# Kernel tuning notes

Measured on AMD Instinct MI355X. Metric: run time of the kernel, lower is better.

Reference implementation:

```python
import jax, jax.numpy as jnp
import numpy as np

N, IN_SIZE, OUT_SIZE = 8192, 256, 64


def setup_inputs() -> dict:
    key = jax.random.key(0)
    kx, kw, kb = jax.random.split(key, 3)
    x = jax.random.normal(kx, (N, IN_SIZE), dtype=jnp.float32)
    # Per-feature Linear(1, out_size): weight w[i] (shape [out_size]) and bias b[i].
    # torch.nn.Linear(1, out_size) init: U(-1, 1) since fan_in = 1.
    W = jax.random.uniform(kw, (IN_SIZE, OUT_SIZE), minval=-1.0, maxval=1.0, dtype=jnp.float32)
    b = jax.random.uniform(kb, (IN_SIZE, OUT_SIZE), minval=-1.0, maxval=1.0, dtype=jnp.float32)
    return {"x": x, "W": W, "b": b}


def reference(x, W, b):
    # x: [N, F]; W, b: [F, D]
    # layer_i(x[:, i:i+1]) = x[:, i, None] * W[i] + b[i]  -> stacked [N, D, F] in torch,
    # here [N, F, D]; mean over feature axis is identical either way.
    out = x[:, :, None] * W[None, :, :] + b[None, :, :]  # [N, F, D]
    out = jnp.nan_to_num(out)
    return out.mean(axis=1)  # [N, D]
```

## Files before the change

kernel.cpp:

```cpp
#include <hip/hip_runtime.h>
#include <stdint.h>

#define NROWS 8192
#define FDIM  256
#define DDIM  64

typedef __attribute__((ext_vector_type(8))) short short8;
typedef __attribute__((ext_vector_type(4))) float floatx4;

__device__ inline unsigned int pack2_bf16(float a, float b) {
    unsigned int ua = __float_as_uint(a);
    unsigned int ub = __float_as_uint(b);
    ua += 0x7fffu + ((ua >> 16) & 1u);
    ub += 0x7fffu + ((ub >> 16) & 1u);
    return (ua >> 16) | (ub & 0xffff0000u);
}

__global__ __launch_bounds__(128)
void nanembed_mfma(const float* __restrict__ x,
                   const float* __restrict__ W,
                   const float* __restrict__ b,
                   float* __restrict__ out)
{
    __shared__ __align__(16) unsigned int bfrag_lds[2048 * 4];
    __shared__ float4 bias_part[8][16];

    const int tid  = threadIdx.x;
    const int lane = tid & 63;
    const int w    = tid >> 6;
    const int q    = lane >> 4;
    const int n    = lane & 15;
    const int r0   = blockIdx.x * 32;

    const int row = r0 + w * 16 + n;
    const float4* xp = reinterpret_cast<const float4*>(x + (size_t)row * FDIM + q * 8);
    float4 xv[16];
    #pragma unroll
    for (int ks = 0; ks < 8; ++ks) {
        xv[2 * ks]     = xp[ks * 8];
        xv[2 * ks + 1] = xp[ks * 8 + 1];
    }

    #pragma unroll
    for (int i = 0; i < 16; ++i) {
        int f  = tid + i * 128;
        int ks = f >> 8;
        int nt = (f >> 6) & 3;
        int fl = f & 63;
        int fq = fl >> 4;
        int c  = nt * 16 + (fl & 15);
        const float* wp = W + (size_t)(ks * 32 + fq * 8) * DDIM + c;
        union { short8 s; unsigned int u[4]; } fr;
        fr.u[0] = pack2_bf16(wp[0 * DDIM], wp[1 * DDIM]);
        fr.u[1] = pack2_bf16(wp[2 * DDIM], wp[3 * DDIM]);
        fr.u[2] = pack2_bf16(wp[4 * DDIM], wp[5 * DDIM]);
        fr.u[3] = pack2_bf16(wp[6 * DDIM], wp[7 * DDIM]);
        reinterpret_cast<short8*>(bfrag_lds)[f] = fr.s;
    }

    {
        const int c4 = tid & 15;
        const int h  = tid >> 4;
        const float4* bp = reinterpret_cast<const float4*>(b) + c4;
        float4 s = make_float4(0.f, 0.f, 0.f, 0.f);
        #pragma unroll 8
        for (int f = h * 32; f < h * 32 + 32; ++f) {
            float4 v = bp[(size_t)f * 16];
            s.x += v.x; s.y += v.y; s.z += v.z; s.w += v.w;
        }
        bias_part[h][c4] = s;
    }

    __syncthreads();

    floatx4 acc[4] = {{0.f, 0.f, 0.f, 0.f}, {0.f, 0.f, 0.f, 0.f},
                      {0.f, 0.f, 0.f, 0.f}, {0.f, 0.f, 0.f, 0.f}};
    #pragma unroll
    for (int ks = 0; ks < 8; ++ks) {
        union { short8 s; unsigned int u[4]; } fa;
        float4 v0 = xv[2 * ks], v1 = xv[2 * ks + 1];
        fa.u[0] = pack2_bf16(v0.x, v0.y);
        fa.u[1] = pack2_bf16(v0.z, v0.w);
        fa.u[2] = pack2_bf16(v1.x, v1.y);
        fa.u[3] = pack2_bf16(v1.z, v1.w);
        #pragma unroll
        for (int nt = 0; nt < 4; ++nt) {
            short8 fb = reinterpret_cast<const short8*>(bfrag_lds)[ks * 256 + nt * 64 + lane];
            acc[nt] = __builtin_amdgcn_mfma_f32_16x16x32_bf16(fa.s, fb, acc[nt], 0, 0, 0);
        }
    }

    #pragma unroll
    for (int nt = 0; nt < 4; ++nt) {
        const int c = nt * 16 + n;
        float bs = 0.f;
        #pragma unroll
        for (int h = 0; h < 8; ++h)
            bs += reinterpret_cast<const float*>(&bias_part[h][0])[c];
        #pragma unroll
        for (int reg = 0; reg < 4; ++reg) {
            const int r = r0 + w * 16 + q * 4 + reg;
            out[(size_t)r * DDIM + c] = (acc[nt][reg] + bs) * (1.0f / 256.0f);
        }
    }
}

extern "C" void kernel_launch(void* const* d_in, const int* in_sizes, int n_in,
                              void* d_out, int out_size, void* d_ws, size_t ws_size,
                              hipStream_t stream) {
    const float* x = (const float*)d_in[0];
    const float* W = (const float*)d_in[1];
    const float* b = (const float*)d_in[2];
    float* out = (float*)d_out;

    nanembed_mfma<<<dim3(NROWS / 32), 128, 0, stream>>>(x, W, b, out);
}
```

Baseline: 65.56 us.

## Split weight packing and bias reduction into a prologue kernel using workspace

```diff
diff --git a/kernel.cpp b/kernel.cpp
--- a/kernel.cpp
+++ b/kernel.cpp
@@ -8,6 +8,7 @@
 typedef __attribute__((ext_vector_type(8))) short short8;
 typedef __attribute__((ext_vector_type(4))) float floatx4;
 
+
 __device__ inline unsigned int pack2_bf16(float a, float b) {
     unsigned int ua = __float_as_uint(a);
     unsigned int ub = __float_as_uint(b);
@@ -17,23 +18,46 @@
 }
 
 __global__ __launch_bounds__(128)
-void nanembed_mfma(const float* __restrict__ x,
-                   const float* __restrict__ W,
+void nanembed_pack(const float* __restrict__ W,
                    const float* __restrict__ b,
-                   float* __restrict__ out)
+                   void* __restrict__ ws)
 {
-    __shared__ __align__(16) unsigned int bfrag_lds[2048 * 4];
-    __shared__ float4 bias_part[8][16];
+    const int bid = blockIdx.x;
+    const int tid = threadIdx.x;
+    if (bid < 16) {
+        const int f  = bid * 128 + tid;
+        const int ks = f >> 8;
+        const int nt = (f >> 6) & 3;
+        const int fl = f & 63;
+        const int fq = fl >> 4;
+        const int c  = nt * 16 + (fl & 15);
+        const float* wp = W + (size_t)(ks * 32 + fq * 8) * DDIM + c;
+        union { short8 s; unsigned int u[4]; } fr;
+        fr.u[0] = pack2_bf16(wp[0 * DDIM], wp[1 * DDIM]);
+        fr.u[1] = pack2_bf16(wp[2 * DDIM], wp[3 * DDIM]);
+        fr.u[2] = pack2_bf16(wp[4 * DDIM], wp[5 * DDIM]);
+        fr.u[3] = pack2_bf16(wp[6 * DDIM], wp[7 * DDIM]);
+        reinterpret_cast<short8*>(ws)[f] = fr.s;
+    } else if (tid < DDIM) {
+        float s = 0.f;
+        #pragma unroll 16
+        for (int f = 0; f < FDIM; ++f)
+            s += b[(size_t)f * DDIM + tid];
+        reinterpret_cast<float*>(ws)[8192 + tid] = s;
+    }
+}
 
-    const int tid  = threadIdx.x;
-    const int lane = tid & 63;
-    const int w    = tid >> 6;
+__global__ __launch_bounds__(64)
+void nanembed_mfma2(const float* __restrict__ x,
+                    const void* __restrict__ ws,
+                    float* __restrict__ out)
+{
+    const int lane = threadIdx.x;
     const int q    = lane >> 4;
     const int n    = lane & 15;
-    const int r0   = blockIdx.x * 32;
+    const int r0   = blockIdx.x * 16;
 
-    const int row = r0 + w * 16 + n;
-    const float4* xp = reinterpret_cast<const float4*>(x + (size_t)row * FDIM + q * 8);
+    const float4* xp = reinterpret_cast<const float4*>(x + (size_t)(r0 + n) * FDIM + q * 8);
     float4 xv[16];
     #pragma unroll
     for (int ks = 0; ks < 8; ++ks) {
@@ -41,37 +65,11 @@
         xv[2 * ks + 1] = xp[ks * 8 + 1];
     }
 
+    const short8* bf   = reinterpret_cast<const short8*>(ws);
+    const float*  bias = reinterpret_cast<const float*>(ws) + 8192;
+    float bsv[4];
     #pragma unroll
-    for (int i = 0; i < 16; ++i) {
-        int f  = tid + i * 128;
-        int ks = f >> 8;
-        int nt = (f >> 6) & 3;
-        int fl = f & 63;
-        int fq = fl >> 4;
-        int c  = nt * 16 + (fl & 15);
-        const float* wp = W + (size_t)(ks * 32 + fq * 8) * DDIM + c;
-        union { short8 s; unsigned int u[4]; } fr;
-        fr.u[0] = pack2_bf16(wp[0 * DDIM], wp[1 * DDIM]);
-        fr.u[1] = pack2_bf16(wp[2 * DDIM], wp[3 * DDIM]);
-        fr.u[2] = pack2_bf16(wp[4 * DDIM], wp[5 * DDIM]);
-        fr.u[3] = pack2_bf16(wp[6 * DDIM], wp[7 * DDIM]);
-        reinterpret_cast<short8*>(bfrag_lds)[f] = fr.s;
-    }
-
-    {
-        const int c4 = tid & 15;
-        const int h  = tid >> 4;
-        const float4* bp = reinterpret_cast<const float4*>(b) + c4;
-        float4 s = make_float4(0.f, 0.f, 0.f, 0.f);
-        #pragma unroll 8
-        for (int f = h * 32; f < h * 32 + 32; ++f) {
-            float4 v = bp[(size_t)f * 16];
-            s.x += v.x; s.y += v.y; s.z += v.z; s.w += v.w;
-        }
-        bias_part[h][c4] = s;
-    }
-
-    __syncthreads();
+    for (int nt = 0; nt < 4; ++nt) bsv[nt] = bias[nt * 16 + n];
 
     floatx4 acc[4] = {{0.f, 0.f, 0.f, 0.f}, {0.f, 0.f, 0.f, 0.f},
                       {0.f, 0.f, 0.f, 0.f}, {0.f, 0.f, 0.f, 0.f}};
@@ -85,7 +83,7 @@
         fa.u[3] = pack2_bf16(v1.z, v1.w);
         #pragma unroll
         for (int nt = 0; nt < 4; ++nt) {
-            short8 fb = reinterpret_cast<const short8*>(bfrag_lds)[ks * 256 + nt * 64 + lane];
+            short8 fb = bf[ks * 256 + nt * 64 + lane];
             acc[nt] = __builtin_amdgcn_mfma_f32_16x16x32_bf16(fa.s, fb, acc[nt], 0, 0, 0);
         }
     }
@@ -93,14 +91,10 @@
     #pragma unroll
     for (int nt = 0; nt < 4; ++nt) {
         const int c = nt * 16 + n;
-        float bs = 0.f;
-        #pragma unroll
-        for (int h = 0; h < 8; ++h)
-            bs += reinterpret_cast<const float*>(&bias_part[h][0])[c];
         #pragma unroll
         for (int reg = 0; reg < 4; ++reg) {
-            const int r = r0 + w * 16 + q * 4 + reg;
-            out[(size_t)r * DDIM + c] = (acc[nt][reg] + bs) * (1.0f / 256.0f);
+            const int r = r0 + q * 4 + reg;
+            out[(size_t)r * DDIM + c] = (acc[nt][reg] + bsv[nt]) * (1.0f / 256.0f);
         }
     }
 }
@@ -113,5 +107,6 @@
     const float* b = (const float*)d_in[2];
     float* out = (float*)d_out;
 
-    nanembed_mfma<<<dim3(NROWS / 32), 128, 0, stream>>>(x, W, b, out);
+    nanembed_pack<<<dim3(17), 128, 0, stream>>>(W, b, d_ws);
+    nanembed_mfma2<<<dim3(NROWS / 16), 64, 0, stream>>>(x, d_ws, out);
 }
```

New measurement: 68.52 us. 1.05x slower.
